# Kernel optimization log

Hardware: AMD Instinct MI355X
Metric: run time of the kernel (lower is better)

The kernel has to match this reference:

```python
import jax, jax.numpy as jnp
import numpy as np
from jax import lax

BN_EPS = 1e-5


def setup_inputs() -> dict:
    key = jax.random.key(0)
    k1, k2 = jax.random.split(key)
    B, C, H, Wd = 32, 256, 56, 56
    x = jax.random.normal(k1, (B, C, H, Wd), dtype=jnp.float32)
    W = jax.random.normal(k2, (C, C, 3, 3), dtype=jnp.float32) * 0.05  # conv weight OIHW
    gamma = jnp.ones((C,), dtype=jnp.float32)
    beta = jnp.zeros((C,), dtype=jnp.float32)
    return {"x": x, "W": W, "gamma": gamma, "beta": beta}


def reference(x, W, gamma, beta):
    # sign activation on input, sign-binarized weights
    s = jnp.sign(x)
    bw = jnp.sign(W)
    # 3x3 conv, stride 1, padding 1 (same spatial size)
    y = lax.conv_general_dilated(
        s, bw,
        window_strides=(1, 1),
        padding=((1, 1), (1, 1)),
        dimension_numbers=("NCHW", "OIHW", "NCHW"),
    )
    # BatchNorm2d in training mode: batch statistics over (N, H, W), biased variance
    mean = jnp.mean(y, axis=(0, 2, 3))
    var = jnp.var(y, axis=(0, 2, 3))
    inv = gamma / jnp.sqrt(var + BN_EPS)
    yn = (y - mean[None, :, None, None]) * inv[None, :, None, None] + beta[None, :, None, None]
    return yn + x
```

## Files before the change

kernel.cpp:

```cpp
#include <hip/hip_runtime.h>
#include <stdint.h>

#define CH 256
#define HWD 56
#define POS (HWD*HWD)
#define BATCH 32
#define NG 4
#define PADW 58
#define PADP (PADW*PADW)

typedef unsigned long long u64;
typedef __attribute__((ext_vector_type(8))) short short8;

__global__ void pack_w_kernel(const float* __restrict__ W, u64* __restrict__ wbits,
                              int* __restrict__ ctap){
    int idx = blockIdx.x*256 + threadIdx.x;
    if (idx >= CH*9) return;
    int o = idx / 9, tap = idx % 9;
    int kh = tap/3, kw = tap%3;
    int totpop = 0;
    for (int g=0; g<4; g++){
        u64 bits = 0;
        for (int j=0; j<64; j++){
            float v = W[((o*CH + g*64 + j)*3 + kh)*3 + kw];
            bits |= (u64)(v >= 0.f) << j;
        }
        wbits[o*36 + tap*4 + g] = bits;
        totpop += __builtin_popcountll(bits);
    }
    ctap[idx] = 256 - 2*totpop;
}

__global__ void pack_x_kernel(const float* __restrict__ x, u64* __restrict__ xpad){
    int idx = blockIdx.x*256 + threadIdx.x;
    if (idx >= BATCH*NG*POS) return;
    int pos = idx % POS;
    int bg  = idx / POS;
    int g = bg & (NG-1);
    int b = bg >> 2;
    const float* xp = x + ((size_t)(b*CH + g*64))*POS + pos;
    u64 bits = 0;
    for (int j=0; j<64; j++){
        float v = xp[(size_t)j*POS];
        bits |= (u64)(v >= 0.f) << j;
    }
    int h = pos / HWD, w = pos % HWD;
    xpad[((size_t)b*PADP + (h+1)*PADW + (w+1))*4 + g] = bits;
}

__global__ __launch_bounds__(448) void conv_kernel(
        const u64* __restrict__ xpad, const u64* __restrict__ wbits,
        const int* __restrict__ ctap,
        short* __restrict__ y16, int* __restrict__ sumI, u64* __restrict__ sumQ){
    int blk = blockIdx.x;
    int b  = blk >> 5;
    int o0 = (blk & 31) * 8;
    int t  = threadIdx.x;
    int w0 = t % HWD;
    int h0 = t / HWD;

    const u64* xb = xpad + (size_t)b*PADP*4 + (size_t)((h0+1)*PADW + (w0+1))*4;

    int acc[7][8];
    #pragma unroll
    for (int k=0;k<7;k++)
        #pragma unroll
        for (int o=0;o<8;o++) acc[k][o]=0;

    #pragma unroll 1
    for (int tap=0; tap<9; ++tap){
        int dh = tap/3 - 1, dw = tap%3 - 1;
        int toff = (dh*PADW + dw)*4;
        u64 wt0[8], wt1[8], wt2[8], wt3[8];
        #pragma unroll
        for (int o=0;o<8;o++){
            const u64* wp = wbits + (size_t)(o0+o)*36 + tap*4;
            wt0[o]=wp[0]; wt1[o]=wp[1]; wt2[o]=wp[2]; wt3[o]=wp[3];
        }
        #pragma unroll
        for (int k=0;k<7;k++){
            const u64* xp = xb + k*(8*PADW*4) + toff;
            u64 xa=xp[0], xc=xp[1], xd=xp[2], xe=xp[3];
            #pragma unroll
            for (int o=0;o<8;o++){
                acc[k][o] += __builtin_popcountll(xa^wt0[o]) + __builtin_popcountll(xc^wt1[o])
                           + __builtin_popcountll(xd^wt2[o]) + __builtin_popcountll(xe^wt3[o]);
            }
        }
    }

    __shared__ int       wls[7][8];
    __shared__ long long wlq[7][8];
    size_t ybase = (size_t)(b*CH + o0)*POS + t;
    bool left  = (w0 == 0);
    bool right = (w0 == HWD-1);
    int wave = t >> 6, lane = t & 63;

    #pragma unroll
    for (int oo=0; oo<8; ++oo){
        const int* cp = ctap + (size_t)(o0+oo)*9;
        int c0=cp[0],c1=cp[1],c2=cp[2],c3=cp[3],c5=cp[5],c6=cp[6],c7=cp[7],c8=cp[8];
        int R0=c0+c1+c2, R2=c6+c7+c8, C0=c0+c3+c6, C2=c2+c5+c8;
        int corrcom = (left?C0:0) + (right?C2:0);
        int topterm = (h0==0) ? (R0 - (left?c0:0) - (right?c2:0)) : 0;
        int botterm = (h0==7) ? (R2 - (left?c6:0) - (right?c8:0)) : 0;
        int ls = 0; long long lq = 0;
        #pragma unroll
        for (int k=0;k<7;k++){
            int y = 2304 - 2*acc[k][oo] - corrcom;
            if (k==0) y -= topterm;
            if (k==6) y -= botterm;
            y16[ybase + (size_t)oo*POS + k*448] = (short)y;
            ls += y;
            lq += (long long)(y*y);
        }
        for (int off=32; off; off>>=1){
            ls += __shfl_down(ls, off);
            lq += __shfl_down(lq, off);
        }
        if (lane == 0){ wls[wave][oo]=ls; wlq[wave][oo]=lq; }
    }
    __syncthreads();
    if (t < 8){
        int bs = 0; long long bq = 0;
        for (int wv=0; wv<7; ++wv){ bs += wls[wv][t]; bq += wlq[wv][t]; }
        atomicAdd(&sumI[o0+t], bs);
        atomicAdd(&sumQ[o0+t], (u64)bq);
    }
}

__global__ void bn_prep_kernel(const int* __restrict__ sumI, const u64* __restrict__ sumQ,
                               const float* __restrict__ gamma, const float* __restrict__ beta,
                               float* __restrict__ invA, float* __restrict__ shiftA){
    int o = threadIdx.x;
    const double N = (double)(BATCH*POS);
    double mean = (double)sumI[o] / N;
    double msq  = (double)sumQ[o] / N;
    double var  = msq - mean*mean;
    double inv  = (double)gamma[o] / sqrt(var + 1e-5);
    invA[o]   = (float)inv;
    shiftA[o] = (float)((double)beta[o] - mean*inv);
}

__global__ void apply_kernel(const short* __restrict__ y16, const float* __restrict__ x,
                             const float* __restrict__ invA, const float* __restrict__ shiftA,
                             float* __restrict__ out){
    int t = blockIdx.x*blockDim.x + threadIdx.x;
    const int total8 = BATCH*CH*POS/8;
    if (t >= total8) return;
    size_t i = (size_t)t*8;
    int c = (t / (POS/8)) & 255;
    short8 yv = *(const short8*)(y16 + i);
    float4 x0 = *(const float4*)(x + i);
    float4 x1 = *(const float4*)(x + i + 4);
    float iv = invA[c], sh = shiftA[c];
    float4 o0, o1;
    o0.x = fmaf((float)yv[0], iv, sh) + x0.x;
    o0.y = fmaf((float)yv[1], iv, sh) + x0.y;
    o0.z = fmaf((float)yv[2], iv, sh) + x0.z;
    o0.w = fmaf((float)yv[3], iv, sh) + x0.w;
    o1.x = fmaf((float)yv[4], iv, sh) + x1.x;
    o1.y = fmaf((float)yv[5], iv, sh) + x1.y;
    o1.z = fmaf((float)yv[6], iv, sh) + x1.z;
    o1.w = fmaf((float)yv[7], iv, sh) + x1.w;
    *(float4*)(out + i)     = o0;
    *(float4*)(out + i + 4) = o1;
}

extern "C" void kernel_launch(void* const* d_in, const int* in_sizes, int n_in,
                              void* d_out, int out_size, void* d_ws, size_t ws_size,
                              hipStream_t stream) {
    const float* x     = (const float*)d_in[0];
    const float* W     = (const float*)d_in[1];
    const float* gamma = (const float*)d_in[2];
    const float* beta  = (const float*)d_in[3];
    float* out = (float*)d_out;

    char* ws = (char*)d_ws;
    short* y16   = (short*)ws;
    u64*   xpad  = (u64*)(ws + 51380224);
    u64*   wbits = (u64*)(ws + 54824960);
    int*   ctap  = (int*)(ws + 54898688);
    int*   sumI  = (int*)(ws + 54907904);
    u64*   sumQ  = (u64*)(ws + 54908928);
    float* invA  = (float*)(ws + 54910976);
    float* shiftA= (float*)(ws + 54912000);

    hipMemsetAsync(xpad, 0, 3444736, stream);
    hipMemsetAsync(sumI, 0, 3072, stream);

    pack_w_kernel<<<9, 256, 0, stream>>>(W, wbits, ctap);
    pack_x_kernel<<<1568, 256, 0, stream>>>(x, xpad);
    conv_kernel<<<BATCH*32, 448, 0, stream>>>(xpad, wbits, ctap, y16, sumI, sumQ);
    bn_prep_kernel<<<1, 256, 0, stream>>>(sumI, sumQ, gamma, beta, invA, shiftA);
    apply_kernel<<<(BATCH*CH*POS/8 + 255)/256, 256, 0, stream>>>(y16, x, invA, shiftA, out);
}
```

Before: 383.5 us.

## Restructure binary conv per-position threading, LDS-transpose x packing, drop pad memset

The conv kernel now uses one output pixel per thread across 8 output channels. Blocks cover 4-row bands, which gives many more, smaller blocks with fewer accumulator registers, and weights are laid out so each output-channel group reads contiguous bits. The x-packing kernel now stages sign bits through swizzled LDS per row and writes the zero padding itself, which removes the separate memset of the padded buffer. The BN statistics reduction moves to LDS plus an xor-shuffle with 32-bit sums. Risks are idle lanes (56 of 64 columns used), more redundant loads per output, and the 32-bit sum of squares coming close to overflow.

```diff
diff --git a/kernel.cpp b/kernel.cpp
--- a/kernel.cpp
+++ b/kernel.cpp
@@ -3,129 +3,161 @@
 
 #define CH 256
 #define HWD 56
-#define POS (HWD*HWD)
+#define POS 3136
 #define BATCH 32
-#define NG 4
 #define PADW 58
 #define PADP (PADW*PADW)
 
 typedef unsigned long long u64;
 typedef __attribute__((ext_vector_type(8))) short short8;
 
-__global__ void pack_w_kernel(const float* __restrict__ W, u64* __restrict__ wbits,
+__global__ void pack_w_kernel(const float* __restrict__ W, u64* __restrict__ wbit8,
                               int* __restrict__ ctap){
     int idx = blockIdx.x*256 + threadIdx.x;
     if (idx >= CH*9) return;
     int o = idx / 9, tap = idx % 9;
     int kh = tap/3, kw = tap%3;
+    int og = o >> 3, oo = o & 7;
     int totpop = 0;
     for (int g=0; g<4; g++){
         u64 bits = 0;
         for (int j=0; j<64; j++){
-            float v = W[((o*CH + g*64 + j)*3 + kh)*3 + kw];
+            float v = W[((size_t)(o*CH + g*64 + j)*3 + kh)*3 + kw];
             bits |= (u64)(v >= 0.f) << j;
         }
-        wbits[o*36 + tap*4 + g] = bits;
+        wbit8[((size_t)(og*9 + tap)*8 + oo)*4 + g] = bits;
         totpop += __builtin_popcountll(bits);
     }
-    ctap[idx] = 256 - 2*totpop;
-}
-
-__global__ void pack_x_kernel(const float* __restrict__ x, u64* __restrict__ xpad){
-    int idx = blockIdx.x*256 + threadIdx.x;
-    if (idx >= BATCH*NG*POS) return;
-    int pos = idx % POS;
-    int bg  = idx / POS;
-    int g = bg & (NG-1);
-    int b = bg >> 2;
-    const float* xp = x + ((size_t)(b*CH + g*64))*POS + pos;
-    u64 bits = 0;
-    for (int j=0; j<64; j++){
-        float v = xp[(size_t)j*POS];
-        bits |= (u64)(v >= 0.f) << j;
-    }
-    int h = pos / HWD, w = pos % HWD;
-    xpad[((size_t)b*PADP + (h+1)*PADW + (w+1))*4 + g] = bits;
-}
-
-__global__ __launch_bounds__(448) void conv_kernel(
-        const u64* __restrict__ xpad, const u64* __restrict__ wbits,
+    ctap[o*9 + tap] = 256 - 2*totpop;
+}
+
+__global__ __launch_bounds__(256) void pack_x_kernel(const float* __restrict__ x, u64* __restrict__ xpad){
+    int blk = blockIdx.x;
+    int rp = blk % 58, b = blk / 58;
+    u64* rowbase = xpad + ((size_t)b*PADP + (size_t)rp*PADW)*4;
+    int t = threadIdx.x;
+    if (rp == 0 || rp == 57){
+        int* ip = (int*)rowbase;
+        for (int j = t; j < PADW*4*2; j += 256) ip[j] = 0;
+        return;
+    }
+    int h = rp - 1;
+    __shared__ char lds[56][256];
+    __shared__ int nib[4][64];
+    int wave = t >> 6, l = t & 63;
+    for (int i = 0; i < 64; ++i){
+        int c = wave*64 + i;
+        if (l < 56){
+            float v = x[((size_t)(b*CH + c))*POS + h*HWD + l];
+            lds[l][c ^ ((l & 31) << 2)] = (v >= 0.f) ? (char)1 : (char)0;
+        }
+    }
+    __syncthreads();
+    for (int i = 0; i < 15; ++i){
+        int p = wave + 4*i;
+        if (p >= 58) break;
+        int val = 0;
+        if (p >= 1 && p <= 56){
+            int w = p - 1;
+            int swz = (w & 31) << 2;
+            const char* lp = lds[w];
+            int b0 = lp[(4*l + 0) ^ swz];
+            int b1 = lp[(4*l + 1) ^ swz];
+            int b2 = lp[(4*l + 2) ^ swz];
+            int b3 = lp[(4*l + 3) ^ swz];
+            val = b0 | (b1<<1) | (b2<<2) | (b3<<3);
+        }
+        nib[wave][l] = val;
+        if (l < 8){
+            int g4 = l & 3;
+            int hi = l >> 2;
+            u64 part = 0;
+            for (int k=0; k<8; ++k){
+                int lane_src = g4*16 + hi*8 + k;
+                part |= (u64)(nib[wave][lane_src] & 0xF) << (4*k);
+            }
+            ((unsigned int*)(rowbase + (size_t)p*4 + g4))[hi] = (unsigned int)part;
+        }
+    }
+}
+
+__global__ __launch_bounds__(256) void conv_kernel(
+        const u64* __restrict__ xpad, const u64* __restrict__ wbit8,
         const int* __restrict__ ctap,
         short* __restrict__ y16, int* __restrict__ sumI, u64* __restrict__ sumQ){
     int blk = blockIdx.x;
-    int b  = blk >> 5;
-    int o0 = (blk & 31) * 8;
-    int t  = threadIdx.x;
-    int w0 = t % HWD;
-    int h0 = t / HWD;
-
-    const u64* xb = xpad + (size_t)b*PADP*4 + (size_t)((h0+1)*PADW + (w0+1))*4;
-
-    int acc[7][8];
+    int og   = blk & 31;
+    int band = (blk >> 5) % 14;
+    int b    = blk / 448;
+    int t = threadIdx.x;
+    int h = band*4 + (t >> 6);
+    int w = t & 63;
+    bool vok = (w < 56);
+    int wc = vok ? w : 55;
+
+    const u64* xb = xpad + ((size_t)b*PADP + (size_t)(h+1)*PADW + (wc+1))*4;
+    const u64* wb = wbit8 + (size_t)og*288;
+
+    int acc[8];
     #pragma unroll
-    for (int k=0;k<7;k++)
-        #pragma unroll
-        for (int o=0;o<8;o++) acc[k][o]=0;
+    for (int i=0;i<8;i++) acc[i] = 0;
 
     #pragma unroll 1
     for (int tap=0; tap<9; ++tap){
         int dh = tap/3 - 1, dw = tap%3 - 1;
-        int toff = (dh*PADW + dw)*4;
-        u64 wt0[8], wt1[8], wt2[8], wt3[8];
+        const u64* xp = xb + (dh*PADW + dw)*4;
+        u64 x0 = xp[0], x1 = xp[1], x2 = xp[2], x3 = xp[3];
+        const u64* wt = wb + tap*32;
         #pragma unroll
-        for (int o=0;o<8;o++){
-            const u64* wp = wbits + (size_t)(o0+o)*36 + tap*4;
-            wt0[o]=wp[0]; wt1[o]=wp[1]; wt2[o]=wp[2]; wt3[o]=wp[3];
-        }
-        #pragma unroll
-        for (int k=0;k<7;k++){
-            const u64* xp = xb + k*(8*PADW*4) + toff;
-            u64 xa=xp[0], xc=xp[1], xd=xp[2], xe=xp[3];
-            #pragma unroll
-            for (int o=0;o<8;o++){
-                acc[k][o] += __builtin_popcountll(xa^wt0[o]) + __builtin_popcountll(xc^wt1[o])
-                           + __builtin_popcountll(xd^wt2[o]) + __builtin_popcountll(xe^wt3[o]);
-            }
-        }
-    }
-
-    __shared__ int       wls[7][8];
-    __shared__ long long wlq[7][8];
-    size_t ybase = (size_t)(b*CH + o0)*POS + t;
-    bool left  = (w0 == 0);
-    bool right = (w0 == HWD-1);
-    int wave = t >> 6, lane = t & 63;
+        for (int oo=0; oo<8; ++oo){
+            acc[oo] += __builtin_popcountll(x0 ^ wt[oo*4+0])
+                     + __builtin_popcountll(x1 ^ wt[oo*4+1])
+                     + __builtin_popcountll(x2 ^ wt[oo*4+2])
+                     + __builtin_popcountll(x3 ^ wt[oo*4+3]);
+        }
+    }
+
+    bool top=(h==0), bot=(h==55), left=(w==0), right=(w==55);
+    int o0 = og*8;
+    __shared__ int sbuf[8][264];
+    __shared__ int qbuf[8][264];
+    size_t ybase = ((size_t)(b*CH + o0)*HWD + h)*HWD + w;
 
     #pragma unroll
     for (int oo=0; oo<8; ++oo){
         const int* cp = ctap + (size_t)(o0+oo)*9;
-        int c0=cp[0],c1=cp[1],c2=cp[2],c3=cp[3],c5=cp[5],c6=cp[6],c7=cp[7],c8=cp[8];
-        int R0=c0+c1+c2, R2=c6+c7+c8, C0=c0+c3+c6, C2=c2+c5+c8;
-        int corrcom = (left?C0:0) + (right?C2:0);
-        int topterm = (h0==0) ? (R0 - (left?c0:0) - (right?c2:0)) : 0;
-        int botterm = (h0==7) ? (R2 - (left?c6:0) - (right?c8:0)) : 0;
-        int ls = 0; long long lq = 0;
+        int corr = 0;
+        if (top)   corr += cp[0]+cp[1]+cp[2];
+        if (bot)   corr += cp[6]+cp[7]+cp[8];
+        if (left)  corr += cp[0]+cp[3]+cp[6];
+        if (right) corr += cp[2]+cp[5]+cp[8];
+        if (top && left)   corr -= cp[0];
+        if (top && right)  corr -= cp[2];
+        if (bot && left)   corr -= cp[6];
+        if (bot && right)  corr -= cp[8];
+        int y = 2304 - 2*acc[oo] - corr;
+        if (vok) y16[ybase + (size_t)oo*POS] = (short)y;
+        sbuf[oo][t] = vok ? y : 0;
+        qbuf[oo][t] = vok ? y*y : 0;
+    }
+    __syncthreads();
+    {
+        int oo = t >> 5, j = t & 31;
+        int ss = 0, qq = 0;
         #pragma unroll
-        for (int k=0;k<7;k++){
-            int y = 2304 - 2*acc[k][oo] - corrcom;
-            if (k==0) y -= topterm;
-            if (k==6) y -= botterm;
-            y16[ybase + (size_t)oo*POS + k*448] = (short)y;
-            ls += y;
-            lq += (long long)(y*y);
-        }
-        for (int off=32; off; off>>=1){
-            ls += __shfl_down(ls, off);
-            lq += __shfl_down(lq, off);
-        }
-        if (lane == 0){ wls[wave][oo]=ls; wlq[wave][oo]=lq; }
-    }
-    __syncthreads();
-    if (t < 8){
-        int bs = 0; long long bq = 0;
-        for (int wv=0; wv<7; ++wv){ bs += wls[wv][t]; bq += wlq[wv][t]; }
-        atomicAdd(&sumI[o0+t], bs);
-        atomicAdd(&sumQ[o0+t], (u64)bq);
+        for (int k=0; k<8; ++k){
+            ss += sbuf[oo][j + 32*k];
+            qq += qbuf[oo][j + 32*k];
+        }
+        #pragma unroll
+        for (int off=1; off<32; off<<=1){
+            ss += __shfl_xor(ss, off);
+            qq += __shfl_xor(qq, off);
+        }
+        if (j == 0){
+            atomicAdd(&sumI[o0+oo], ss);
+            atomicAdd(&sumQ[o0+oo], (u64)(unsigned)qq);
+        }
     }
 }
 
@@ -179,19 +211,18 @@
     char* ws = (char*)d_ws;
     short* y16   = (short*)ws;
     u64*   xpad  = (u64*)(ws + 51380224);
-    u64*   wbits = (u64*)(ws + 54824960);
+    u64*   wbit8 = (u64*)(ws + 54824960);
     int*   ctap  = (int*)(ws + 54898688);
     int*   sumI  = (int*)(ws + 54907904);
     u64*   sumQ  = (u64*)(ws + 54908928);
     float* invA  = (float*)(ws + 54910976);
     float* shiftA= (float*)(ws + 54912000);
 
-    hipMemsetAsync(xpad, 0, 3444736, stream);
     hipMemsetAsync(sumI, 0, 3072, stream);
 
-    pack_w_kernel<<<9, 256, 0, stream>>>(W, wbits, ctap);
-    pack_x_kernel<<<1568, 256, 0, stream>>>(x, xpad);
-    conv_kernel<<<BATCH*32, 448, 0, stream>>>(xpad, wbits, ctap, y16, sumI, sumQ);
+    pack_w_kernel<<<9, 256, 0, stream>>>(W, wbit8, ctap);
+    pack_x_kernel<<<BATCH*58, 256, 0, stream>>>(x, xpad);
+    conv_kernel<<<BATCH*32*14, 256, 0, stream>>>(xpad, wbit8, ctap, y16, sumI, sumQ);
     bn_prep_kernel<<<1, 256, 0, stream>>>(sumI, sumQ, gamma, beta, invA, shiftA);
     apply_kernel<<<(BATCH*CH*POS/8 + 255)/256, 256, 0, stream>>>(y16, x, invA, shiftA, out);
 }
```

Result: slower. 414.4 us (+8.0%).
